# Performance work log

Measured on AMD Instinct MI355X. Metric: run time of the kernel, lower is better.

Reference implementation:

```python
import jax, jax.numpy as jnp
import numpy as np

# Module constants (match init_kwargs)
C = 384            # dim
NUM_DILATION = 3
DILATIONS = (1, 2, 3)
KS = 3             # kernel_size
HEADS_INNER = 2    # = qk_scale passed positionally as inner num_heads
SCALE = 2.0        # scale = qk_scale (truthy int), exactly as the torch code computes
B, H, W = 2, 128, 128


def _windows(x, dil, H, W):
    """Zero-padded dilated 3x3 neighborhood gather (== F.unfold with padding=dil).
    x: (B,H,W,d) -> (B,H,W,d,9), kernel taps ordered row-major (kh, kw)."""
    xp = jnp.pad(x, ((0, 0), (dil, dil), (dil, dil), (0, 0)))
    taps = [xp[:, i * dil:i * dil + H, j * dil:j * dil + W, :]
            for i in range(KS) for j in range(KS)]
    return jnp.stack(taps, axis=-1)


def _dilate_attention(q, k, v, dil):
    """q,k,v: (B,H,W,d) with d = C/num_dilation. Per-pixel 3x3 dilated window attention."""
    Bq, Hq, Wq, d = q.shape
    hd = d // HEADS_INNER
    kwin = _windows(k, dil, Hq, Wq).reshape(Bq, Hq, Wq, HEADS_INNER, hd, KS * KS)
    vwin = _windows(v, dil, Hq, Wq).reshape(Bq, Hq, Wq, HEADS_INNER, hd, KS * KS)
    qh = q.reshape(Bq, Hq, Wq, HEADS_INNER, hd)
    logits = jnp.einsum('bxyhd,bxyhdk->bxyhk', qh, kwin) * SCALE
    attn = jax.nn.softmax(logits, axis=-1)
    out = jnp.einsum('bxyhk,bxyhdk->bxyhd', attn, vwin)  # (B,H,W,h,hd)
    return out.reshape(Bq, Hq, Wq, d)


def setup_inputs() -> dict:
    key = jax.random.key(0)
    ks = jax.random.split(key, 8)
    s = 0.02
    return {
        'mov': jax.random.normal(ks[0], (B, H, W, C), jnp.float32),
        'fix': jax.random.normal(ks[1], (B, H, W, C), jnp.float32),
        'Wm_qkv': jax.random.normal(ks[2], (3 * C, C), jnp.float32) * s,
        'Wf_qkv': jax.random.normal(ks[3], (3 * C, C), jnp.float32) * s,
        'Wm_proj': jax.random.normal(ks[4], (C, C), jnp.float32) * s,
        'bm_proj': jnp.zeros((C,), jnp.float32),
        'Wf_proj': jax.random.normal(ks[5], (C, C), jnp.float32) * s,
        'bf_proj': jnp.zeros((C,), jnp.float32),
    }


def reference(mov, fix, Wm_qkv, Wf_qkv, Wm_proj, bm_proj, Wf_proj, bf_proj):
    Bq, Hq, Wq, Cq = mov.shape
    d = Cq // NUM_DILATION
    # 1x1 conv qkv (no bias). Output channels ordered (3, num_dilation, d), as in torch reshape.
    mq = jnp.einsum('bxyc,oc->bxyo', mov, Wm_qkv).reshape(Bq, Hq, Wq, 3, NUM_DILATION, d)
    fq = jnp.einsum('bxyc,oc->bxyo', fix, Wf_qkv).reshape(Bq, Hq, Wq, 3, NUM_DILATION, d)
    m_res, f_res = [], []
    for i, dil in enumerate(DILATIONS):
        # cross attention: mov branch queries with fix's q over mov's k/v, and vice versa
        m_res.append(_dilate_attention(fq[..., 0, i, :], mq[..., 1, i, :], mq[..., 2, i, :], dil))
        f_res.append(_dilate_attention(mq[..., 0, i, :], fq[..., 1, i, :], fq[..., 2, i, :], dil))
    mov_o = jnp.stack(m_res, axis=3).reshape(Bq, Hq, Wq, Cq)
    fix_o = jnp.stack(f_res, axis=3).reshape(Bq, Hq, Wq, Cq)
    mov_o = mov_o @ Wm_proj.T + bm_proj
    fix_o = fix_o @ Wf_proj.T + bf_proj
    return mov_o, fix_o
```

## Files before the change

kernel.cpp:

```cpp
#include <hip/hip_runtime.h>
#include <hip/hip_bf16.h>

#define PPIX 32768
#define K384 384

typedef __attribute__((ext_vector_type(8))) short s16x8;
typedef __attribute__((ext_vector_type(4))) float f32x4;

__device__ __forceinline__ float bf2f(short u) {
  union { unsigned int i; float f; } c;
  c.i = ((unsigned int)(unsigned short)u) << 16;
  return c.f;
}

__device__ __forceinline__ unsigned short f2b(float x) {
  union { float f; unsigned int i; } c; c.f = x;
  unsigned int u = c.i;
  return (unsigned short)((u + 0x7fffu + ((u >> 16) & 1u)) >> 16);
}

__global__ __launch_bounds__(256) void cvt_all(
    const float* __restrict__ s0, unsigned short* __restrict__ d0,
    const float* __restrict__ s1, unsigned short* __restrict__ d1,
    const float* __restrict__ s2, unsigned short* __restrict__ d2,
    const float* __restrict__ s3, unsigned short* __restrict__ d3,
    const float* __restrict__ s4, unsigned short* __restrict__ d4,
    const float* __restrict__ s5, unsigned short* __restrict__ d5) {
  int b = blockIdx.x;
  const float* s; unsigned short* d; int rb;
  if      (b < 6144)  { s = s0; d = d0; rb = b; }
  else if (b < 12288) { s = s1; d = d1; rb = b - 6144; }
  else if (b < 12504) { s = s2; d = d2; rb = b - 12288; }
  else if (b < 12720) { s = s3; d = d3; rb = b - 12504; }
  else if (b < 12792) { s = s4; d = d4; rb = b - 12720; }
  else                { s = s5; d = d5; rb = b - 12792; }
  int i = rb * 256 + threadIdx.x;
  const float4* in4 = (const float4*)s;
  float4 a = in4[(size_t)i * 2], c4 = in4[(size_t)i * 2 + 1];
  s16x8 r;
  r[0] = (short)f2b(a.x);  r[1] = (short)f2b(a.y);  r[2] = (short)f2b(a.z);  r[3] = (short)f2b(a.w);
  r[4] = (short)f2b(c4.x); r[5] = (short)f2b(c4.y); r[6] = (short)f2b(c4.z); r[7] = (short)f2b(c4.w);
  *(s16x8*)(d + (size_t)i * 8) = r;
}

__device__ __forceinline__ void async_ld16(const void* g, void* l) {
  __builtin_amdgcn_global_load_lds(
      (const __attribute__((address_space(1))) unsigned int*)g,
      (__attribute__((address_space(3))) unsigned int*)l, 16, 0, 0);
}

template<int N, bool F32OUT>
__global__ __launch_bounds__(256) void gemm_bt(
    const unsigned short* __restrict__ A0, const unsigned short* __restrict__ A1,
    const unsigned short* __restrict__ B0, const unsigned short* __restrict__ B1,
    void* __restrict__ C0v, void* __restrict__ C1v,
    const float* __restrict__ bias0, const float* __restrict__ bias1) {
  const int bm = blockIdx.x, bn = blockIdx.y, bz = blockIdx.z;
  const unsigned short* A = bz ? A1 : A0;
  const unsigned short* Bm = bz ? B1 : B0;
  const int tid = threadIdx.x;
  const int wid = tid >> 6, lane = tid & 63;
  __shared__ unsigned short lds[2][128 * 64];
  unsigned short* ldsA = lds[0];
  unsigned short* ldsB = lds[1];
  f32x4 acc[4][4] = {};
  const int wm = wid >> 1, wn = wid & 1;
  const int srow = tid >> 3;
  const int scol = (tid & 7) * 8;
  const int r = lane & 15, q2 = lane >> 4;

  for (int kt = 0; kt < K384 / 64; ++kt) {
    const int k0 = kt * 64;
#pragma unroll
    for (int j = 0; j < 4; ++j) {
      async_ld16(A + (size_t)(bm * 128 + j * 32 + srow) * K384 + k0 + scol,
                 (char*)ldsA + (j * 32 + wid * 8) * 128);
      async_ld16(Bm + (size_t)(bn * 128 + j * 32 + srow) * K384 + k0 + scol,
                 (char*)ldsB + (j * 32 + wid * 8) * 128);
    }
    __syncthreads();
#pragma unroll
    for (int ks = 0; ks < 2; ++ks) {
      s16x8 af[4], bf[4];
#pragma unroll
      for (int mi = 0; mi < 4; ++mi)
        af[mi] = *(const s16x8*)&ldsA[(wm * 64 + mi * 16 + r) * 64 + ks * 32 + q2 * 8];
#pragma unroll
      for (int ni = 0; ni < 4; ++ni)
        bf[ni] = *(const s16x8*)&ldsB[(wn * 64 + ni * 16 + r) * 64 + ks * 32 + q2 * 8];
#pragma unroll
      for (int mi = 0; mi < 4; ++mi)
#pragma unroll
        for (int ni = 0; ni < 4; ++ni)
          acc[mi][ni] = __builtin_amdgcn_mfma_f32_16x16x32_bf16(af[mi], bf[ni], acc[mi][ni], 0, 0, 0);
    }
    __syncthreads();
  }

  unsigned short* slice = &lds[wid >> 1][(wid & 1) * 4096];

  if constexpr (!F32OUT) {
    unsigned short* C = (unsigned short*)(bz ? C1v : C0v);
#pragma unroll
    for (int mi = 0; mi < 4; ++mi)
#pragma unroll
      for (int ni = 0; ni < 4; ++ni)
#pragma unroll
        for (int rr = 0; rr < 4; ++rr)
          slice[(mi * 16 + q2 * 4 + rr) * 64 + ni * 16 + r] = f2b(acc[mi][ni][rr]);
    asm volatile("s_waitcnt lgkmcnt(0)" ::: "memory");
    const size_t cbase = (size_t)(bm * 128 + wm * 64) * N + bn * 128 + wn * 64;
#pragma unroll
    for (int c = 0; c < 8; ++c) {
      const int gr = c * 8 + (lane >> 3), gc = (lane & 7) * 8;
      s16x8 v = *(const s16x8*)&slice[c * 512 + lane * 8];
      *(s16x8*)&C[cbase + (size_t)gr * N + gc] = v;
    }
  } else {
    float* C = (float*)(bz ? C1v : C0v);
    const float* bias = bz ? bias1 : bias0;
    float* sliceF = (float*)slice;
#pragma unroll
    for (int p = 0; p < 2; ++p) {
      asm volatile("s_waitcnt lgkmcnt(0)" ::: "memory");
#pragma unroll
      for (int mi2 = 0; mi2 < 2; ++mi2) {
        const int mi = p * 2 + mi2;
#pragma unroll
        for (int ni = 0; ni < 4; ++ni) {
          const float bv = bias[bn * 128 + wn * 64 + ni * 16 + r];
#pragma unroll
          for (int rr = 0; rr < 4; ++rr)
            sliceF[(mi2 * 16 + q2 * 4 + rr) * 64 + ni * 16 + r] = acc[mi][ni][rr] + bv;
        }
      }
      asm volatile("s_waitcnt lgkmcnt(0)" ::: "memory");
#pragma unroll
      for (int c = 0; c < 8; ++c) {
        const int rr2 = c * 4 + (lane >> 4), gc = (lane & 15) * 4;
        float4 v = *(const float4*)&sliceF[rr2 * 64 + gc];
        *(float4*)&C[(size_t)(bm * 128 + wm * 64 + p * 32 + rr2) * N + bn * 128 + wn * 64 + gc] = v;
      }
    }
  }
}

__global__ __launch_bounds__(256) void dilate_attn8(
    const unsigned short* __restrict__ qkv_m, const unsigned short* __restrict__ qkv_f,
    unsigned short* __restrict__ att_m, unsigned short* __restrict__ att_f) {
  const int t = blockIdx.x * 256 + threadIdx.x;
  const int lane8 = t & 7;
  const int g = t >> 3;
  const int pix = g & 32767;
  const int rest = g >> 15;
  const int branch = rest >= 6;
  const int ih = branch ? rest - 6 : rest;
  const int i = ih >> 1, h = ih & 1;
  const int dil = i + 1;
  const int x = pix & 127, y = (pix >> 7) & 127, b = pix >> 14;
  const unsigned short* qsrc  = branch ? qkv_m : qkv_f;
  const unsigned short* kvsrc = branch ? qkv_f : qkv_m;
  unsigned short* dst = branch ? att_f : att_m;
  const int co = i * 128 + h * 64 + lane8 * 8;

  float qf[8];
  {
    s16x8 v = *(const s16x8*)(qsrc + (size_t)pix * 1152 + co);
#pragma unroll
    for (int e = 0; e < 8; ++e) qf[e] = bf2f(v[e]);
  }

  float lg[9];
  s16x8 vk[9];
#pragma unroll
  for (int tt = 0; tt < 9; ++tt) {
    const int ky = y + (tt / 3 - 1) * dil;
    const int kx = x + (tt % 3 - 1) * dil;
    s16x8 kk;
#pragma unroll
    for (int e = 0; e < 8; ++e) { kk[e] = 0; vk[tt][e] = 0; }
    if ((unsigned)ky < 128u && (unsigned)kx < 128u) {
      const unsigned short* p = kvsrc + (size_t)((b << 14) + (ky << 7) + kx) * 1152 + co;
      kk = *(const s16x8*)(p + 384);
      vk[tt] = *(const s16x8*)(p + 768);
    }
    float s = 0.f;
#pragma unroll
    for (int e = 0; e < 8; ++e) s += qf[e] * bf2f(kk[e]);
    s += __shfl_xor(s, 1, 8);
    s += __shfl_xor(s, 2, 8);
    s += __shfl_xor(s, 4, 8);
    lg[tt] = s * 2.0f;
  }

  float mx = lg[0];
#pragma unroll
  for (int tt = 1; tt < 9; ++tt) mx = fmaxf(mx, lg[tt]);
  float den = 0.f, w[9];
#pragma unroll
  for (int tt = 0; tt < 9; ++tt) { w[tt] = __expf(lg[tt] - mx); den += w[tt]; }
  const float inv = 1.f / den;

  float out[8];
#pragma unroll
  for (int e = 0; e < 8; ++e) out[e] = 0.f;
#pragma unroll
  for (int tt = 0; tt < 9; ++tt) {
    const float wt = w[tt] * inv;
#pragma unroll
    for (int e = 0; e < 8; ++e) out[e] += wt * bf2f(vk[tt][e]);
  }

  s16x8 rv;
#pragma unroll
  for (int e = 0; e < 8; ++e) rv[e] = (short)f2b(out[e]);
  *(s16x8*)(dst + (size_t)pix * 384 + co) = rv;
}

extern "C" void kernel_launch(void* const* d_in, const int* in_sizes, int n_in,
                              void* d_out, int out_size, void* d_ws, size_t ws_size,
                              hipStream_t stream) {
  const float* mov     = (const float*)d_in[0];
  const float* fixp    = (const float*)d_in[1];
  const float* Wm_qkv  = (const float*)d_in[2];
  const float* Wf_qkv  = (const float*)d_in[3];
  const float* Wm_proj = (const float*)d_in[4];
  const float* bm_proj = (const float*)d_in[5];
  const float* Wf_proj = (const float*)d_in[6];
  const float* bf_proj = (const float*)d_in[7];

  char* ws = (char*)d_ws;
  unsigned short* xm    = (unsigned short*)(ws);
  unsigned short* xf    = (unsigned short*)(ws + 25165824);
  unsigned short* wqm   = (unsigned short*)(ws + 50331648);
  unsigned short* wqf   = (unsigned short*)(ws + 51216384);
  unsigned short* wpm   = (unsigned short*)(ws + 52101120);
  unsigned short* wpf   = (unsigned short*)(ws + 52396032);
  unsigned short* qkv_m = (unsigned short*)(ws + 52690944);
  unsigned short* qkv_f = (unsigned short*)(ws + 128188416);
  unsigned short* att_m = (unsigned short*)(ws + 203685888);
  unsigned short* att_f = (unsigned short*)(ws + 228851712);

  cvt_all<<<12864, 256, 0, stream>>>(mov, xm, fixp, xf, Wm_qkv, wqm,
                                     Wf_qkv, wqf, Wm_proj, wpm, Wf_proj, wpf);

  gemm_bt<1152, false><<<dim3(256, 9, 2), 256, 0, stream>>>(
      xm, xf, wqm, wqf, qkv_m, qkv_f, nullptr, nullptr);

  dilate_attn8<<<12288, 256, 0, stream>>>(qkv_m, qkv_f, att_m, att_f);

  gemm_bt<384, true><<<dim3(256, 3, 2), 256, 0, stream>>>(
      att_m, att_f, wpm, wpf,
      (float*)d_out, (float*)d_out + 12582912, bm_proj, bf_proj);
}
```

Baseline: 389.7 us.

## Use 256x256-tile double-buffered QKV GEMM with swizzled LDS and padded output

Replaces the 128x128 QKV projection GEMM with a dedicated 512-thread kernel. It computes 256x256 tiles, double-buffers async global-to-LDS loads, and XOR-swizzles LDS to avoid bank conflicts. N is padded from 1152 to 1280 by zero-filling the extra weight rows in the convert kernel, so the tiles divide evenly. The attention output buffers now reuse the bf16 input buffers, which shrinks the workspace. The padding adds about 11% wasted GEMM work, and the kernel's 128KB of LDS per block limits how many blocks can be resident.

```diff
diff --git a/kernel.cpp b/kernel.cpp
--- a/kernel.cpp
+++ b/kernel.cpp
@@ -1,8 +1,8 @@
 #include <hip/hip_runtime.h>
 #include <hip/hip_bf16.h>
 
-#define PPIX 32768
 #define K384 384
+#define NP   1280
 
 typedef __attribute__((ext_vector_type(8))) short s16x8;
 typedef __attribute__((ext_vector_type(4))) float f32x4;
@@ -27,6 +27,13 @@
     const float* __restrict__ s4, unsigned short* __restrict__ d4,
     const float* __restrict__ s5, unsigned short* __restrict__ d5) {
   int b = blockIdx.x;
+  if (b >= 12864) {
+    unsigned short* d = (b < 12888) ? d2 : d3;
+    int i = (b - ((b < 12888) ? 12864 : 12888)) * 256 + threadIdx.x;
+    s16x8 z = {};
+    *(s16x8*)(d + 442368 + (size_t)i * 8) = z;
+    return;
+  }
   const float* s; unsigned short* d; int rb;
   if      (b < 6144)  { s = s0; d = d0; rb = b; }
   else if (b < 12288) { s = s1; d = d1; rb = b - 6144; }
@@ -49,11 +56,105 @@
       (__attribute__((address_space(3))) unsigned int*)l, 16, 0, 0);
 }
 
-template<int N, bool F32OUT>
-__global__ __launch_bounds__(256) void gemm_bt(
+__global__ __launch_bounds__(512, 2) void gemm_qkv256(
     const unsigned short* __restrict__ A0, const unsigned short* __restrict__ A1,
     const unsigned short* __restrict__ B0, const unsigned short* __restrict__ B1,
-    void* __restrict__ C0v, void* __restrict__ C1v,
+    unsigned short* __restrict__ C0, unsigned short* __restrict__ C1) {
+  const int bm = blockIdx.x, bn = blockIdx.y, bz = blockIdx.z;
+  const unsigned short* A = bz ? A1 : A0;
+  const unsigned short* B = bz ? B1 : B0;
+  unsigned short* C = bz ? C1 : C0;
+  const int tid = threadIdx.x;
+  const int w = tid >> 6, lane = tid & 63;
+  const int wm = w >> 2, wn = w & 3;
+  const int r_ = lane & 15, q2 = lane >> 4;
+  __shared__ unsigned short L[65536];
+
+  f32x4 acc[8][4] = {};
+
+  const int rlo = (tid >> 3) & 7;
+  const int sc = ((lane & 7) ^ rlo) * 8;
+  const size_t arow0 = (size_t)bm * 256;
+  const size_t brow0 = (size_t)bn * 256;
+
+  auto STAGE = [&](int kt, int b01) {
+    const int k0 = kt * 64;
+#pragma unroll
+    for (int j = 0; j < 4; ++j) {
+      const int rr = j * 64 + w * 8;
+      async_ld16(A + (arow0 + rr + rlo) * K384 + k0 + sc,
+                 (char*)L + (size_t)(b01 * 16384 + rr * 64) * 2);
+      async_ld16(B + (brow0 + rr + rlo) * K384 + k0 + sc,
+                 (char*)L + (size_t)(32768 + b01 * 16384 + rr * 64) * 2);
+    }
+  };
+
+  auto COMPUTE = [&](int b01) {
+    const unsigned short* bufA = L + b01 * 16384;
+    const unsigned short* bufB = L + 32768 + b01 * 16384;
+#pragma unroll
+    for (int ks = 0; ks < 2; ++ks) {
+      s16x8 af[8], bf[4];
+#pragma unroll
+      for (int mi = 0; mi < 8; ++mi) {
+        const int row = wm * 128 + mi * 16 + r_;
+        const int c = (ks * 4 + q2) ^ (r_ & 7);
+        af[mi] = *(const s16x8*)&bufA[row * 64 + c * 8];
+      }
+#pragma unroll
+      for (int ni = 0; ni < 4; ++ni) {
+        const int row = wn * 64 + ni * 16 + r_;
+        const int c = (ks * 4 + q2) ^ (r_ & 7);
+        bf[ni] = *(const s16x8*)&bufB[row * 64 + c * 8];
+      }
+#pragma unroll
+      for (int mi = 0; mi < 8; ++mi)
+#pragma unroll
+        for (int ni = 0; ni < 4; ++ni)
+          acc[mi][ni] = __builtin_amdgcn_mfma_f32_16x16x32_bf16(af[mi], bf[ni], acc[mi][ni], 0, 0, 0);
+    }
+  };
+
+  STAGE(0, 0);
+  STAGE(1, 1);
+#pragma unroll
+  for (int kt = 0; kt < 6; ++kt) {
+    if (kt < 5) { asm volatile("s_waitcnt vmcnt(8)" ::: "memory"); }
+    else        { asm volatile("s_waitcnt vmcnt(0)" ::: "memory"); }
+    __builtin_amdgcn_s_barrier();
+    __builtin_amdgcn_sched_barrier(0);
+    COMPUTE(kt & 1);
+    __builtin_amdgcn_sched_barrier(0);
+    __builtin_amdgcn_s_barrier();
+    __builtin_amdgcn_sched_barrier(0);
+    if (kt + 2 < 6) STAGE(kt + 2, kt & 1);
+  }
+  __builtin_amdgcn_s_barrier();
+
+  unsigned short* slice = L + w * 8192;
+#pragma unroll
+  for (int mi = 0; mi < 8; ++mi)
+#pragma unroll
+    for (int ni = 0; ni < 4; ++ni)
+#pragma unroll
+      for (int rr2 = 0; rr2 < 4; ++rr2)
+        slice[(mi * 16 + q2 * 4 + rr2) * 64 + ni * 16 + r_] = f2b(acc[mi][ni][rr2]);
+  asm volatile("s_waitcnt lgkmcnt(0)" ::: "memory");
+  __builtin_amdgcn_sched_barrier(0);
+  const size_t crow0 = (size_t)(bm * 256 + wm * 128);
+  const int ccol0 = bn * 256 + wn * 64;
+#pragma unroll
+  for (int c = 0; c < 16; ++c) {
+    s16x8 v = *(const s16x8*)&slice[c * 512 + lane * 8];
+    *(s16x8*)&C[(crow0 + c * 8 + (lane >> 3)) * NP + ccol0 + (lane & 7) * 8] = v;
+  }
+}
+
+template<int N>
+__global__ __launch_bounds__(256) void gemm_proj(
+    const unsigned short* __restrict__ A0, const unsigned short* __restrict__ A1,
+    const unsigned short* __restrict__ B0, const unsigned short* __restrict__ B1,
+    float* __restrict__ C0, float* __restrict__ C1,
     const float* __restrict__ bias0, const float* __restrict__ bias1) {
   const int bm = blockIdx.x, bn = blockIdx.y, bz = blockIdx.z;
   const unsigned short* A = bz ? A1 : A0;
@@ -97,50 +198,30 @@
     __syncthreads();
   }
 
+  float* C = bz ? C1 : C0;
+  const float* bias = bz ? bias1 : bias0;
   unsigned short* slice = &lds[wid >> 1][(wid & 1) * 4096];
-
-  if constexpr (!F32OUT) {
-    unsigned short* C = (unsigned short*)(bz ? C1v : C0v);
-#pragma unroll
-    for (int mi = 0; mi < 4; ++mi)
-#pragma unroll
-      for (int ni = 0; ni < 4; ++ni)
+  float* sliceF = (float*)slice;
+#pragma unroll
+  for (int p = 0; p < 2; ++p) {
+    asm volatile("s_waitcnt lgkmcnt(0)" ::: "memory");
+#pragma unroll
+    for (int mi2 = 0; mi2 < 2; ++mi2) {
+      const int mi = p * 2 + mi2;
+#pragma unroll
+      for (int ni = 0; ni < 4; ++ni) {
+        const float bv = bias[bn * 128 + wn * 64 + ni * 16 + r];
 #pragma unroll
         for (int rr = 0; rr < 4; ++rr)
-          slice[(mi * 16 + q2 * 4 + rr) * 64 + ni * 16 + r] = f2b(acc[mi][ni][rr]);
+          sliceF[(mi2 * 16 + q2 * 4 + rr) * 64 + ni * 16 + r] = acc[mi][ni][rr] + bv;
+      }
+    }
     asm volatile("s_waitcnt lgkmcnt(0)" ::: "memory");
-    const size_t cbase = (size_t)(bm * 128 + wm * 64) * N + bn * 128 + wn * 64;
 #pragma unroll
     for (int c = 0; c < 8; ++c) {
-      const int gr = c * 8 + (lane >> 3), gc = (lane & 7) * 8;
-      s16x8 v = *(const s16x8*)&slice[c * 512 + lane * 8];
-      *(s16x8*)&C[cbase + (size_t)gr * N + gc] = v;
-    }
-  } else {
-    float* C = (float*)(bz ? C1v : C0v);
-    const float* bias = bz ? bias1 : bias0;
-    float* sliceF = (float*)slice;
-#pragma unroll
-    for (int p = 0; p < 2; ++p) {
-      asm volatile("s_waitcnt lgkmcnt(0)" ::: "memory");
-#pragma unroll
-      for (int mi2 = 0; mi2 < 2; ++mi2) {
-        const int mi = p * 2 + mi2;
-#pragma unroll
-        for (int ni = 0; ni < 4; ++ni) {
-          const float bv = bias[bn * 128 + wn * 64 + ni * 16 + r];
-#pragma unroll
-          for (int rr = 0; rr < 4; ++rr)
-            sliceF[(mi2 * 16 + q2 * 4 + rr) * 64 + ni * 16 + r] = acc[mi][ni][rr] + bv;
-        }
-      }
-      asm volatile("s_waitcnt lgkmcnt(0)" ::: "memory");
-#pragma unroll
-      for (int c = 0; c < 8; ++c) {
-        const int rr2 = c * 4 + (lane >> 4), gc = (lane & 15) * 4;
-        float4 v = *(const float4*)&sliceF[rr2 * 64 + gc];
-        *(float4*)&C[(size_t)(bm * 128 + wm * 64 + p * 32 + rr2) * N + bn * 128 + wn * 64 + gc] = v;
-      }
+      const int rr2 = c * 4 + (lane >> 4), gc = (lane & 15) * 4;
+      float4 v = *(const float4*)&sliceF[rr2 * 64 + gc];
+      *(float4*)&C[(size_t)(bm * 128 + wm * 64 + p * 32 + rr2) * N + bn * 128 + wn * 64 + gc] = v;
     }
   }
 }
@@ -165,7 +246,7 @@
 
   float qf[8];
   {
-    s16x8 v = *(const s16x8*)(qsrc + (size_t)pix * 1152 + co);
+    s16x8 v = *(const s16x8*)(qsrc + (size_t)pix * NP + co);
 #pragma unroll
     for (int e = 0; e < 8; ++e) qf[e] = bf2f(v[e]);
   }
@@ -180,7 +261,7 @@
 #pragma unroll
     for (int e = 0; e < 8; ++e) { kk[e] = 0; vk[tt][e] = 0; }
     if ((unsigned)ky < 128u && (unsigned)kx < 128u) {
-      const unsigned short* p = kvsrc + (size_t)((b << 14) + (ky << 7) + kx) * 1152 + co;
+      const unsigned short* p = kvsrc + (size_t)((b << 14) + (ky << 7) + kx) * NP + co;
       kk = *(const s16x8*)(p + 384);
       vk[tt] = *(const s16x8*)(p + 768);
     }
@@ -196,9 +277,9 @@
   float mx = lg[0];
 #pragma unroll
   for (int tt = 1; tt < 9; ++tt) mx = fmaxf(mx, lg[tt]);
-  float den = 0.f, w[9];
-#pragma unroll
-  for (int tt = 0; tt < 9; ++tt) { w[tt] = __expf(lg[tt] - mx); den += w[tt]; }
+  float den = 0.f, wgt[9];
+#pragma unroll
+  for (int tt = 0; tt < 9; ++tt) { wgt[tt] = __expf(lg[tt] - mx); den += wgt[tt]; }
   const float inv = 1.f / den;
 
   float out[8];
@@ -206,7 +287,7 @@
   for (int e = 0; e < 8; ++e) out[e] = 0.f;
 #pragma unroll
   for (int tt = 0; tt < 9; ++tt) {
-    const float wt = w[tt] * inv;
+    const float wt = wgt[tt] * inv;
 #pragma unroll
     for (int e = 0; e < 8; ++e) out[e] += wt * bf2f(vk[tt][e]);
   }
@@ -232,24 +313,23 @@
   char* ws = (char*)d_ws;
   unsigned short* xm    = (unsigned short*)(ws);
   unsigned short* xf    = (unsigned short*)(ws + 25165824);
+  unsigned short* att_m = xm;
+  unsigned short* att_f = xf;
   unsigned short* wqm   = (unsigned short*)(ws + 50331648);
-  unsigned short* wqf   = (unsigned short*)(ws + 51216384);
-  unsigned short* wpm   = (unsigned short*)(ws + 52101120);
-  unsigned short* wpf   = (unsigned short*)(ws + 52396032);
-  unsigned short* qkv_m = (unsigned short*)(ws + 52690944);
-  unsigned short* qkv_f = (unsigned short*)(ws + 128188416);
-  unsigned short* att_m = (unsigned short*)(ws + 203685888);
-  unsigned short* att_f = (unsigned short*)(ws + 228851712);
-
-  cvt_all<<<12864, 256, 0, stream>>>(mov, xm, fixp, xf, Wm_qkv, wqm,
+  unsigned short* wqf   = (unsigned short*)(ws + 51314688);
+  unsigned short* wpm   = (unsigned short*)(ws + 52297728);
+  unsigned short* wpf   = (unsigned short*)(ws + 52592640);
+  unsigned short* qkv_m = (unsigned short*)(ws + 52887552);
+  unsigned short* qkv_f = (unsigned short*)(ws + 136773632);
+
+  cvt_all<<<12912, 256, 0, stream>>>(mov, xm, fixp, xf, Wm_qkv, wqm,
                                      Wf_qkv, wqf, Wm_proj, wpm, Wf_proj, wpf);
 
-  gemm_bt<1152, false><<<dim3(256, 9, 2), 256, 0, stream>>>(
-      xm, xf, wqm, wqf, qkv_m, qkv_f, nullptr, nullptr);
+  gemm_qkv256<<<dim3(128, 5, 2), 512, 0, stream>>>(xm, xf, wqm, wqf, qkv_m, qkv_f);
 
   dilate_attn8<<<12288, 256, 0, stream>>>(qkv_m, qkv_f, att_m, att_f);
 
-  gemm_bt<384, true><<<dim3(256, 3, 2), 256, 0, stream>>>(
+  gemm_proj<384><<<dim3(256, 3, 2), 256, 0, stream>>>(
       att_m, att_f, wpm, wpf,
       (float*)d_out, (float*)d_out + 12582912, bm_proj, bf_proj);
 }
```

Result: faster. 363.3 us (-6.8%).
